# Performance work log

Hardware: AMD Instinct MI355X
Metric: run time of the kernel (lower is better)

The kernel has to match this reference:

```python
import jax, jax.numpy as jnp
import numpy as np

B = 8388608  # batch of 2-angle inputs


def setup_inputs() -> dict:
    key = jax.random.key(0)
    k1, k2 = jax.random.split(key)
    x = jax.random.normal(k1, (B, 2), dtype=jnp.float32) * jnp.pi
    # trainable RY rotation angle (tq.RY(has_params=True, trainable=True))
    theta = jax.random.uniform(k2, (1,), dtype=jnp.float32, minval=0.0, maxval=2.0 * np.pi)
    return {"x": x, "theta": theta}


def reference(x, theta):
    # --- encoder: RY(x0) on q0, RY(x1) on q1, starting from |00> ---
    half = x * 0.5
    c = jnp.cos(half)  # [B,2]
    s = jnp.sin(half)  # [B,2]
    a0 = jnp.stack([c[:, 0], s[:, 0]], axis=-1)  # q0 amplitudes [B,2]
    a1 = jnp.stack([c[:, 1], s[:, 1]], axis=-1)  # q1 amplitudes [B,2]
    # state[b, i, j] = amplitude of |i j>, real-valued (RY/CNOT are real)
    state = a0[:, :, None] * a1[:, None, :]  # [B,2,2]

    # --- CNOT(control=q0, target=q1): flip target where control = 1 ---
    state = jnp.stack([state[:, 0, :], state[:, 1, ::-1]], axis=1)

    # --- trainable RY(theta) on q0 ---
    th = theta[0] * 0.5
    ct, st = jnp.cos(th), jnp.sin(th)
    ry = jnp.stack([jnp.stack([ct, -st]), jnp.stack([st, ct])])  # [2,2]
    state = jnp.einsum('ij,bjk->bik', ry, state)

    # --- measure <Z0>, <Z1> ---
    p = state * state  # probabilities [B,2,2]
    z0 = p[:, 0, :].sum(-1) - p[:, 1, :].sum(-1)
    z1 = p[:, :, 0].sum(-1) - p[:, :, 1].sum(-1)
    z = jnp.stack([z0, z1], axis=-1)  # [B,2]
    return (z + 1.0) * 0.5
```

## Files before the change

### kernel.cpp

```cpp
#include <hip/hip_runtime.h>


__global__ __launch_bounds__(256) void qc_kernel(
    const float4* __restrict__ x4,
    const float* __restrict__ theta,
    float4* __restrict__ out4,
    int n4)
{
    int i = blockIdx.x * blockDim.x + threadIdx.x;
    if (i >= n4) return;

    float th = theta[0];
    float ct = __cosf(th);
    float st = __sinf(th);

    float4 v = x4[i];

    float s0 = __sinf(v.x), c0 = __cosf(v.x);
    float s1 = __sinf(v.y), c1 = __cosf(v.y);
    float s2 = __sinf(v.z), c2 = __cosf(v.z);
    float s3 = __sinf(v.w), c3 = __cosf(v.w);

    float4 o;
    o.x = 0.5f * (1.0f + ct * c0 - st * s0 * s1);
    o.y = 0.5f * (1.0f + c0 * c1);
    o.z = 0.5f * (1.0f + ct * c2 - st * s2 * s3);
    o.w = 0.5f * (1.0f + c2 * c3);

    out4[i] = o;
}

extern "C" void kernel_launch(void* const* d_in, const int* in_sizes, int n_in,
                              void* d_out, int out_size, void* d_ws, size_t ws_size,
                              hipStream_t stream) {
    const float* x     = (const float*)d_in[0];
    const float* theta = (const float*)d_in[1];
    float* out         = (float*)d_out;

    int n  = in_sizes[0];
    int n4 = n / 4;

    const int block = 256;
    int grid = (n4 + block - 1) / block;

    qc_kernel<<<grid, block, 0, stream>>>(
        (const float4*)x, theta, (float4*)out, n4);
}
```

Baseline: 110.2 us.

## Use product-to-sum cosines and grid-stride loop with four loads in flight

Rewrites the sin/cos products as sums of cosines of angle sums and differences, dropping from eight transcendental calls to six per float4. The launch is capped at 2048 blocks and each thread walks a grid-stride loop with four independent float4 loads issued before compute, aiming for more memory-level parallelism per thread. The identity rewrite changes rounding slightly, and the capped grid may lower occupancy on a memory-bound kernel.

```diff
diff --git a/kernel.cpp b/kernel.cpp
--- a/kernel.cpp
+++ b/kernel.cpp
@@ -1,5 +1,20 @@
 #include <hip/hip_runtime.h>
 
+
+__device__ __forceinline__ float4 qc_elem(float4 v, float ct, float st) {
+    float c0  = __cosf(v.x);
+    float cu0 = __cosf(v.x + v.y);
+    float cv0 = __cosf(v.x - v.y);
+    float c1  = __cosf(v.z);
+    float cu1 = __cosf(v.z + v.w);
+    float cv1 = __cosf(v.z - v.w);
+    float4 o;
+    o.x = 0.5f + 0.5f * ct * c0 - 0.25f * st * (cv0 - cu0);
+    o.y = 0.5f + 0.25f * (cu0 + cv0);
+    o.z = 0.5f + 0.5f * ct * c1 - 0.25f * st * (cv1 - cu1);
+    o.w = 0.5f + 0.25f * (cu1 + cv1);
+    return o;
+}
 
 __global__ __launch_bounds__(256) void qc_kernel(
     const float4* __restrict__ x4,
@@ -7,27 +22,31 @@
     float4* __restrict__ out4,
     int n4)
 {
-    int i = blockIdx.x * blockDim.x + threadIdx.x;
-    if (i >= n4) return;
+    int tid = blockIdx.x * blockDim.x + threadIdx.x;
+    int T   = gridDim.x * blockDim.x;
 
     float th = theta[0];
     float ct = __cosf(th);
     float st = __sinf(th);
 
-    float4 v = x4[i];
-
-    float s0 = __sinf(v.x), c0 = __cosf(v.x);
-    float s1 = __sinf(v.y), c1 = __cosf(v.y);
-    float s2 = __sinf(v.z), c2 = __cosf(v.z);
-    float s3 = __sinf(v.w), c3 = __cosf(v.w);
-
-    float4 o;
-    o.x = 0.5f * (1.0f + ct * c0 - st * s0 * s1);
-    o.y = 0.5f * (1.0f + c0 * c1);
-    o.z = 0.5f * (1.0f + ct * c2 - st * s2 * s3);
-    o.w = 0.5f * (1.0f + c2 * c3);
-
-    out4[i] = o;
+    int i = tid;
+    for (; i + 3 * T < n4; i += 4 * T) {
+        float4 a = x4[i];
+        float4 b = x4[i + T];
+        float4 c = x4[i + 2 * T];
+        float4 d = x4[i + 3 * T];
+        float4 oa = qc_elem(a, ct, st);
+        float4 ob = qc_elem(b, ct, st);
+        float4 oc = qc_elem(c, ct, st);
+        float4 od = qc_elem(d, ct, st);
+        out4[i]         = oa;
+        out4[i + T]     = ob;
+        out4[i + 2 * T] = oc;
+        out4[i + 3 * T] = od;
+    }
+    for (; i < n4; i += T) {
+        out4[i] = qc_elem(x4[i], ct, st);
+    }
 }
 
 extern "C" void kernel_launch(void* const* d_in, const int* in_sizes, int n_in,
@@ -42,6 +61,7 @@
 
     const int block = 256;
     int grid = (n4 + block - 1) / block;
+    if (grid > 2048) grid = 2048;
 
     qc_kernel<<<grid, block, 0, stream>>>(
         (const float4*)x, theta, (float4*)out, n4);
```

After: 114.6 us. 1.04x slower.
